# Kernel optimization log

Measured on AMD Instinct MI355X. Metric: run time of the kernel, lower is better.

The kernel has to match this reference:

```python
import jax, jax.numpy as jnp
import numpy as np

SAMPLING_RATE = 48000
HARMONIC_NUM = 8
DIM = HARMONIC_NUM + 1
SINE_AMP = 0.1
NOISE_STD = 0.003
VOICED_THRESHOLD = 0.0


def setup_inputs() -> dict:
    key = jax.random.key(0)
    B, T = 4, 480000
    # realistic voiced pitch contour in [80, 400) Hz
    f0 = jax.random.uniform(key, (B, T, 1), dtype=jnp.float32, minval=80.0, maxval=400.0)
    return {"f0": f0}


def reference(f0):
    B, T, _ = f0.shape
    # harmonic stack: f0_buf[:, :, k] = f0 * (k+1)   -> [B, T, DIM]
    harmonics = jnp.arange(1, DIM + 1, dtype=f0.dtype)
    f0_buf = f0 * harmonics  # broadcast [B,T,1] * [DIM]

    # normalized phase increment per sample
    rad_values = (f0_buf / SAMPLING_RATE) % 1.0

    # random initial phase per (batch, harmonic); fundamental gets phase 0
    k_ini, k_noise = jax.random.split(jax.random.key(42))
    rand_ini = jax.random.uniform(k_ini, (B, DIM), dtype=f0.dtype)
    rand_ini = rand_ini.at[:, 0].set(0.0)
    rad_values = rad_values.at[:, 0, :].add(rand_ini)

    # phase-unwrap correction: detect wrap points of cumsum % 1 and subtract 1
    tmp_over_one = jnp.cumsum(rad_values, axis=1) % 1.0
    wrap = (tmp_over_one[:, 1:, :] - tmp_over_one[:, :-1, :]) < 0  # [B,T-1,DIM]
    cumsum_shift = jnp.concatenate(
        [jnp.zeros((B, 1, DIM), dtype=f0.dtype), -wrap.astype(f0.dtype)], axis=1
    )

    phase = jnp.cumsum(rad_values + cumsum_shift, axis=1) * (2.0 * jnp.pi)
    sine_waves = jnp.sin(phase) * SINE_AMP  # [B,T,DIM]

    # voiced/unvoiced mask from fundamental f0
    uv = (f0 > VOICED_THRESHOLD).astype(f0.dtype)  # [B,T,1]

    noise_amp = uv * NOISE_STD + (1.0 - uv) * (SINE_AMP / 3.0)
    noise = jax.random.normal(k_noise, sine_waves.shape, dtype=f0.dtype)
    return sine_waves * uv + noise_amp * noise
```

## Files before the change

### kernel.cpp

```cpp
#include <hip/hip_runtime.h>
#include <math.h>
#include <stdint.h>

#pragma clang fp contract(off)

#define BB   4
#define TT   480000
#define DIM  9
#define TILE 256
#define NTT  1875

#define PARTITIONABLE 1

__host__ __device__ static inline void threefry2x32(uint32_t k0, uint32_t k1,
                                                    uint32_t x0, uint32_t x1,
                                                    uint32_t& o0, uint32_t& o1) {
  const uint32_t ks2 = k0 ^ k1 ^ 0x1BD11BDAu;
  x0 += k0; x1 += k1;
#define TF_R(r) { x0 += x1; x1 = (x1 << (r)) | (x1 >> (32 - (r))); x1 ^= x0; }
  TF_R(13) TF_R(15) TF_R(26) TF_R(6)
  x0 += k1;  x1 += ks2 + 1u;
  TF_R(17) TF_R(29) TF_R(16) TF_R(24)
  x0 += ks2; x1 += k0 + 2u;
  TF_R(13) TF_R(15) TF_R(26) TF_R(6)
  x0 += k0;  x1 += k1 + 3u;
  TF_R(17) TF_R(29) TF_R(16) TF_R(24)
  x0 += k1;  x1 += ks2 + 4u;
  TF_R(13) TF_R(15) TF_R(26) TF_R(6)
  x0 += ks2; x1 += k0 + 5u;
#undef TF_R
  o0 = x0; o1 = x1;
}

__device__ __forceinline__ float fracf_(float x) { return x - truncf(x); }

__device__ __forceinline__ float u01_(uint32_t bits) {
  return __uint_as_float((bits >> 9) | 0x3f800000u) - 1.0f;
}

__device__ static inline float erfinv_xla(float x) {
  float t = (1.0f - x) * (1.0f + x);
  float w = -0.6931471805599453f * __builtin_amdgcn_logf(t);
  float p;
  if (w < 5.0f) {
    w = w - 2.5f;
    p = 2.81022636e-08f;
    p = 3.43273939e-07f  + p * w;
    p = -3.5233877e-06f  + p * w;
    p = -4.39150654e-06f + p * w;
    p = 0.00021858087f   + p * w;
    p = -0.00125372503f  + p * w;
    p = -0.00417768164f  + p * w;
    p = 0.246640727f     + p * w;
    p = 1.50140941f      + p * w;
  } else {
    w = __builtin_amdgcn_sqrtf(w) - 3.0f;
    p = -0.000200214257f;
    p = 0.000100950558f  + p * w;
    p = 0.00134934322f   + p * w;
    p = -0.00367342844f  + p * w;
    p = 0.00573950773f   + p * w;
    p = -0.0076224613f   + p * w;
    p = 0.00943887047f   + p * w;
    p = 1.00167406f      + p * w;
    p = 2.83297682f      + p * w;
  }
  return p * x;
}

__device__ __forceinline__ float nrm_(uint32_t bits) {
  const float LO = -0.9999999403953552f;
  float u = u01_(bits) * 2.0f + LO;
  u = fmaxf(LO, u);
  return 1.4142135623730951f * erfinv_xla(u);
}

__device__ __forceinline__ uint32_t ri_bits(uint32_t kk0, uint32_t kk1, uint32_t j) {
  uint32_t o0, o1;
#if PARTITIONABLE
  threefry2x32(kk0, kk1, 0u, j, o0, o1);
  return o0 ^ o1;
#else
  if (j < 18u) { threefry2x32(kk0, kk1, j, j + 18u, o0, o1); return o0; }
  threefry2x32(kk0, kk1, j - 18u, j, o0, o1); return o1;
#endif
}

__device__ __forceinline__ uint32_t noise_bits(uint32_t kn0, uint32_t kn1, uint32_t i) {
  uint32_t o0, o1;
#if PARTITIONABLE
  threefry2x32(kn0, kn1, 0u, i, o0, o1);
  return o0 ^ o1;
#else
  const uint32_t half = 2u * TT * DIM;
  if (i < half) { threefry2x32(kn0, kn1, i, i + half, o0, o1); return o0; }
  threefry2x32(kn0, kn1, i - half, i, o0, o1); return o1;
#endif
}

__device__ __forceinline__ float rand_ini_val(uint32_t ki0, uint32_t ki1, int b, int k) {
  if (k == 0) return 0.0f;
  return u01_(ri_bits(ki0, ki1, (uint32_t)(b * DIM + k)));
}

struct Tree { float n1a, n1b, Mv[6]; };

__device__ __forceinline__ void build_tree4(float x0, float x1, float x2, float x3,
                                            Tree& T, int l) {
  T.n1a = x0 + x1;
  T.n1b = x2 + x3;
  T.Mv[0] = T.n1a + T.n1b;
#pragma unroll
  for (int s = 1; s < 6; ++s)
    T.Mv[s] = __shfl(T.Mv[s - 1], 2 * l) + __shfl(T.Mv[s - 1], 2 * l + 1);
}
__device__ __forceinline__ float tile_sum4(const Tree& T) {
  return __shfl(T.Mv[5], 0) + __shfl(T.Mv[5], 1);
}
__device__ __forceinline__ float fold4(const Tree& T, int n, float carry) {
  float acc = carry;
#pragma unroll
  for (int b = 7; b >= 2; --b) {
    float t = __shfl(T.Mv[b - 2], (n >> (b + 1)) << 1);
    acc = ((n >> b) & 1) ? acc + t : acc;
  }
  if (n & 2) acc = acc + T.n1a;
  return acc;
}

__global__ __launch_bounds__(256) void k_up1(const float* __restrict__ f0,
                                             float* __restrict__ gL,
                                             uint32_t ki0, uint32_t ki1) {
  int task = blockIdx.x * 4 + (threadIdx.x >> 6);
  int l = threadIdx.x & 63;
  int b = task / NTT, j = task - b * NTT;
  float4 f4 = *(const float4*)(f0 + (size_t)b * TT + j * TILE + 4 * l);
  const float RINV = 1.0f / 48000.0f;
  float rb0 = f4.x * RINV, rb1 = f4.y * RINV, rb2 = f4.z * RINV, rb3 = f4.w * RINV;
  bool ini = (j == 0) & (l == 0);
#pragma unroll
  for (int k = 0; k < DIM; ++k) {
    float h = (float)(k + 1);
    float r0 = fracf_(rb0 * h), r1 = fracf_(rb1 * h);
    float r2 = fracf_(rb2 * h), r3 = fracf_(rb3 * h);
    if (ini) r0 = r0 + rand_ini_val(ki0, ki1, b, k);
    Tree T; build_tree4(r0, r1, r2, r3, T, l);
    float ts = tile_sum4(T);
    if (l == 0) gL[(b * DIM + k) * NTT + j] = ts;
  }
}

__global__ __launch_bounds__(256) void k_midscan(float* __restrict__ gbuf) {
  const int NLEV = 11;
  const int SZ[11]  = {1875, 937, 468, 234, 117, 58, 29, 14, 7, 3, 1};
  const int OFF[11] = {0, 1875, 2812, 3280, 3514, 3631, 3689, 3718, 3732, 3739, 3742};
  __shared__ float buf[3743];
  float* g = gbuf + (size_t)blockIdx.x * NTT;
  int tid = threadIdx.x;
  float tmp[8];
#pragma unroll
  for (int u = 0; u < 8; ++u) { int i = tid + u * 256; tmp[u] = (i < NTT) ? g[i] : 0.0f; }
#pragma unroll
  for (int u = 0; u < 8; ++u) { int i = tid + u * 256; if (i < NTT) buf[i] = tmp[u]; }
  __syncthreads();
#pragma unroll
  for (int lv = 0; lv + 1 < NLEV; ++lv) {
    int m = SZ[lv + 1];
    const float* src = buf + OFF[lv];
    float* dst = buf + OFF[lv + 1];
    for (int i = tid; i < m; i += 256) dst[i] = src[2 * i] + src[2 * i + 1];
    __syncthreads();
  }
#pragma unroll
  for (int lv = NLEV - 2; lv >= 0; --lv) {
    int n = SZ[lv], m = SZ[lv + 1];
    float* cur = buf + OFF[lv];
    const float* up = buf + OFF[lv + 1];
    for (int i = tid; i < m; i += 256) {
      float s = up[i];
      cur[2 * i + 1] = s;
      if (2 * i + 2 < n) cur[2 * i + 2] = s + cur[2 * i + 2];
    }
    __syncthreads();
  }
#pragma unroll
  for (int u = 0; u < 8; ++u) { int i = tid + u * 256; if (i < NTT) g[i] = buf[i]; }
}

__global__ __launch_bounds__(256) void k_d1u2(const float* __restrict__ f0,
                                              const float* __restrict__ gS1,
                                              float* __restrict__ gL2,
                                              ulonglong2* __restrict__ wrapw,
                                              uint32_t ki0, uint32_t ki1) {
  int task = blockIdx.x * 4 + (threadIdx.x >> 6);
  int l = threadIdx.x & 63;
  int b = task / NTT, j = task - b * NTT;
  float4 f4 = *(const float4*)(f0 + (size_t)b * TT + j * TILE + 4 * l);
  const float RINV = 1.0f / 48000.0f;
  float rb0 = f4.x * RINV, rb1 = f4.y * RINV, rb2 = f4.z * RINV, rb3 = f4.w * RINV;
  bool ini = (j == 0) & (l == 0);
  bool notfirst = (j > 0) | (l > 0);
#pragma unroll
  for (int k = 0; k < DIM; ++k) {
    float h = (float)(k + 1);
    float r0 = fracf_(rb0 * h), r1 = fracf_(rb1 * h);
    float r2 = fracf_(rb2 * h), r3 = fracf_(rb3 * h);
    if (ini) r0 = r0 + rand_ini_val(ki0, ki1, b, k);
    Tree T; build_tree4(r0, r1, r2, r3, T, l);
    int base = (b * DIM + k) * NTT;
    float C = (j > 0) ? gS1[base + j - 1] : 0.0f;
    float S = gS1[base + j];
    float c3 = fold4(T, 4 * l + 4, C);
    c3 = (l == 63) ? S : c3;
    float c1 = fold4(T, 4 * l + 2, C);
    float cp = __shfl_up(c3, 1);
    if (l == 0) cp = C;
    float c0 = cp + r0;
    float c2 = c1 + r2;
    float fp = fracf_(cp), g0 = fracf_(c0), g1 = fracf_(c1);
    float g2 = fracf_(c2), g3 = fracf_(c3);
    bool w0 = notfirst & (g0 < fp);
    bool w1 = g1 < g0;
    bool w2 = g2 < g1;
    bool w3 = g3 < g2;
    float y0 = w0 ? r0 - 1.0f : r0, y1 = w1 ? r1 - 1.0f : r1;
    float y2 = w2 ? r2 - 1.0f : r2, y3 = w3 ? r3 - 1.0f : r3;
    unsigned long long m0 = __ballot(w0), m1 = __ballot(w1);
    unsigned long long m2 = __ballot(w2), m3 = __ballot(w3);
    Tree Ty; build_tree4(y0, y1, y2, y3, Ty, l);
    float ts = tile_sum4(Ty);
    if (l == 0) {
      gL2[base + j] = ts;
      wrapw[2 * (base + j)]     = make_ulonglong2(m0, m1);
      wrapw[2 * (base + j) + 1] = make_ulonglong2(m2, m3);
    }
  }
}

__global__ __launch_bounds__(256) void k_d2out(const float* __restrict__ f0,
                                               const float* __restrict__ gS2,
                                               const ulonglong2* __restrict__ wrapw,
                                               float* __restrict__ out,
                                               uint32_t ki0, uint32_t ki1,
                                               uint32_t kn0, uint32_t kn1) {
  int task = blockIdx.x * 4 + (threadIdx.x >> 6);
  int l = threadIdx.x & 63;
  int b = task / NTT, j = task - b * NTT;
  int t0 = j * TILE + 4 * l;
  float4 f4 = *(const float4*)(f0 + (size_t)b * TT + t0);
  const float RINV = 1.0f / 48000.0f;
  float rb0 = f4.x * RINV, rb1 = f4.y * RINV, rb2 = f4.z * RINV, rb3 = f4.w * RINV;
  bool ini = (j == 0) & (l == 0);
  float uv0 = (f4.x > 0.0f) ? 1.0f : 0.0f, uv1 = (f4.y > 0.0f) ? 1.0f : 0.0f;
  float uv2 = (f4.z > 0.0f) ? 1.0f : 0.0f, uv3 = (f4.w > 0.0f) ? 1.0f : 0.0f;
  const float AMP3 = 0.0333333333333333333f;
  float na0 = uv0 * 0.003f + (1.0f - uv0) * AMP3;
  float na1 = uv1 * 0.003f + (1.0f - uv1) * AMP3;
  float na2 = uv2 * 0.003f + (1.0f - uv2) * AMP3;
  float na3 = uv3 * 0.003f + (1.0f - uv3) * AMP3;
  float ob[36];
#pragma unroll
  for (int k = 0; k < DIM; ++k) {
    float h = (float)(k + 1);
    float r0 = fracf_(rb0 * h), r1 = fracf_(rb1 * h);
    float r2 = fracf_(rb2 * h), r3 = fracf_(rb3 * h);
    if (ini) r0 = r0 + rand_ini_val(ki0, ki1, b, k);
    int base = (b * DIM + k) * NTT;
    ulonglong2 wA = wrapw[2 * (base + j)];
    ulonglong2 wB = wrapw[2 * (base + j) + 1];
    float y0 = ((wA.x >> l) & 1ull) ? r0 - 1.0f : r0;
    float y1 = ((wA.y >> l) & 1ull) ? r1 - 1.0f : r1;
    float y2 = ((wB.x >> l) & 1ull) ? r2 - 1.0f : r2;
    float y3 = ((wB.y >> l) & 1ull) ? r3 - 1.0f : r3;
    Tree T; build_tree4(y0, y1, y2, y3, T, l);
    float C2 = (j > 0) ? gS2[base + j - 1] : 0.0f;
    float S2 = gS2[base + j];
    float d3 = fold4(T, 4 * l + 4, C2);
    d3 = (l == 63) ? S2 : d3;
    float d1 = fold4(T, 4 * l + 2, C2);
    float dp = __shfl_up(d3, 1);
    if (l == 0) dp = C2;
    float d0 = dp + y0;
    float d2 = d1 + y2;
    float s0 = __builtin_amdgcn_sinf(d0) * 0.1f;
    float s1 = __builtin_amdgcn_sinf(d1) * 0.1f;
    float s2 = __builtin_amdgcn_sinf(d2) * 0.1f;
    float s3 = __builtin_amdgcn_sinf(d3) * 0.1f;
    uint32_t fi = (uint32_t)(b * TT + t0) * (uint32_t)DIM + (uint32_t)k;
    float n0 = nrm_(noise_bits(kn0, kn1, fi));
    float n1 = nrm_(noise_bits(kn0, kn1, fi + 9u));
    float n2 = nrm_(noise_bits(kn0, kn1, fi + 18u));
    float n3 = nrm_(noise_bits(kn0, kn1, fi + 27u));
    ob[k]      = s0 * uv0 + na0 * n0;
    ob[9 + k]  = s1 * uv1 + na1 * n1;
    ob[18 + k] = s2 * uv2 + na2 * n2;
    ob[27 + k] = s3 * uv3 + na3 * n3;
  }
  float4* po = (float4*)(out + ((size_t)b * TT + t0) * DIM);
#pragma unroll
  for (int q = 0; q < 9; ++q)
    po[q] = make_float4(ob[4 * q], ob[4 * q + 1], ob[4 * q + 2], ob[4 * q + 3]);
}

extern "C" void kernel_launch(void* const* d_in, const int* in_sizes, int n_in,
                              void* d_out, int out_size, void* d_ws, size_t ws_size,
                              hipStream_t stream) {
  (void)in_sizes; (void)n_in; (void)out_size; (void)ws_size;
  const float* f0 = (const float*)d_in[0];
  float* out = (float*)d_out;
  float* gBuf1 = (float*)d_ws;
  float* gBuf2 = gBuf1 + 36 * NTT;
  ulonglong2* wrapw =
      (ulonglong2*)((char*)d_ws + (size_t)2 * 36 * NTT * sizeof(float));

  uint32_t ki0, ki1, kn0, kn1;
#if PARTITIONABLE
  threefry2x32(0u, 42u, 0u, 0u, ki0, ki1);
  threefry2x32(0u, 42u, 0u, 1u, kn0, kn1);
#else
  uint32_t a0, a1, b0, b1;
  threefry2x32(0u, 42u, 0u, 2u, a0, a1);
  threefry2x32(0u, 42u, 1u, 3u, b0, b1);
  ki0 = a0; ki1 = b0;
  kn0 = a1; kn1 = b1;
#endif

  k_up1    <<<(BB * NTT) / 4, 256, 0, stream>>>(f0, gBuf1, ki0, ki1);
  k_midscan<<<36, 256, 0, stream>>>(gBuf1);
  k_d1u2   <<<(BB * NTT) / 4, 256, 0, stream>>>(f0, gBuf1, gBuf2, wrapw, ki0, ki1);
  k_midscan<<<36, 256, 0, stream>>>(gBuf2);
  k_d2out  <<<(BB * NTT) / 4, 256, 0, stream>>>(f0, gBuf2, wrapw, out,
                                                ki0, ki1, kn0, kn1);
}
```

Measured before the change: 197.4 us.

## Stage output through LDS for coalesced stores and use wave-per-row midscan

The output kernel now writes each wave's 256×9 results into padded shared memory and then stores them as contiguous float4 runs across lanes. Before, each lane wrote 36 consecutive floats, which gave strided per-lane stores. The mid-level scan now gives one wave per row (9 blocks of 4 waves instead of 36 blocks), which removes block-wide barriers. Scalar readfirstlane indexing and an inline v_cndmask that consumes the wrap bitmask directly as an SGPR lane mask shorten the wrap-bit select. The trade-offs are more LDS use per block in the output kernel and fewer workgroups in the scan, and the wave-synchronous scan leans on lockstep wave execution without any barrier.

```diff
diff --git a/kernel.cpp b/kernel.cpp
--- a/kernel.cpp
+++ b/kernel.cpp
@@ -103,6 +103,12 @@
   return u01_(ri_bits(ki0, ki1, (uint32_t)(b * DIM + k)));
 }
 
+__device__ __forceinline__ float selbit(unsigned long long m, float aFalse, float bTrue) {
+  float r;
+  asm("v_cndmask_b32 %0, %1, %2, %3" : "=v"(r) : "v"(aFalse), "v"(bTrue), "s"(m));
+  return r;
+}
+
 struct Tree { float n1a, n1b, Mv[6]; };
 
 __device__ __forceinline__ void build_tree4(float x0, float x1, float x2, float x3,
@@ -154,37 +160,31 @@
   const int NLEV = 11;
   const int SZ[11]  = {1875, 937, 468, 234, 117, 58, 29, 14, 7, 3, 1};
   const int OFF[11] = {0, 1875, 2812, 3280, 3514, 3631, 3689, 3718, 3732, 3739, 3742};
-  __shared__ float buf[3743];
-  float* g = gbuf + (size_t)blockIdx.x * NTT;
-  int tid = threadIdx.x;
-  float tmp[8];
-#pragma unroll
-  for (int u = 0; u < 8; ++u) { int i = tid + u * 256; tmp[u] = (i < NTT) ? g[i] : 0.0f; }
-#pragma unroll
-  for (int u = 0; u < 8; ++u) { int i = tid + u * 256; if (i < NTT) buf[i] = tmp[u]; }
-  __syncthreads();
+  __shared__ float buf[4][3743];
+  int w = threadIdx.x >> 6, l = threadIdx.x & 63;
+  int row = blockIdx.x * 4 + w;
+  float* g = gbuf + (size_t)row * NTT;
+  float* s = buf[w];
+  for (int i = l; i < NTT; i += 64) s[i] = g[i];
 #pragma unroll
   for (int lv = 0; lv + 1 < NLEV; ++lv) {
     int m = SZ[lv + 1];
-    const float* src = buf + OFF[lv];
-    float* dst = buf + OFF[lv + 1];
-    for (int i = tid; i < m; i += 256) dst[i] = src[2 * i] + src[2 * i + 1];
-    __syncthreads();
+    const float* src = s + OFF[lv];
+    float* dst = s + OFF[lv + 1];
+    for (int i = l; i < m; i += 64) dst[i] = src[2 * i] + src[2 * i + 1];
   }
 #pragma unroll
   for (int lv = NLEV - 2; lv >= 0; --lv) {
     int n = SZ[lv], m = SZ[lv + 1];
-    float* cur = buf + OFF[lv];
-    const float* up = buf + OFF[lv + 1];
-    for (int i = tid; i < m; i += 256) {
-      float s = up[i];
-      cur[2 * i + 1] = s;
-      if (2 * i + 2 < n) cur[2 * i + 2] = s + cur[2 * i + 2];
+    float* cur = s + OFF[lv];
+    const float* up = s + OFF[lv + 1];
+    for (int i = l; i < m; i += 64) {
+      float ss = up[i];
+      cur[2 * i + 1] = ss;
+      if (2 * i + 2 < n) cur[2 * i + 2] = ss + cur[2 * i + 2];
     }
-    __syncthreads();
-  }
-#pragma unroll
-  for (int u = 0; u < 8; ++u) { int i = tid + u * 256; if (i < NTT) g[i] = buf[i]; }
+  }
+  for (int i = l; i < NTT; i += 64) g[i] = s[i];
 }
 
 __global__ __launch_bounds__(256) void k_d1u2(const float* __restrict__ f0,
@@ -207,9 +207,9 @@
     float r2 = fracf_(rb2 * h), r3 = fracf_(rb3 * h);
     if (ini) r0 = r0 + rand_ini_val(ki0, ki1, b, k);
     Tree T; build_tree4(r0, r1, r2, r3, T, l);
-    int base = (b * DIM + k) * NTT;
-    float C = (j > 0) ? gS1[base + j - 1] : 0.0f;
-    float S = gS1[base + j];
+    int bju = __builtin_amdgcn_readfirstlane((b * DIM + k) * NTT + j);
+    float S = gS1[bju];
+    float C = (j > 0) ? gS1[bju - 1] : 0.0f;
     float c3 = fold4(T, 4 * l + 4, C);
     c3 = (l == 63) ? S : c3;
     float c1 = fold4(T, 4 * l + 2, C);
@@ -230,9 +230,9 @@
     Tree Ty; build_tree4(y0, y1, y2, y3, Ty, l);
     float ts = tile_sum4(Ty);
     if (l == 0) {
-      gL2[base + j] = ts;
-      wrapw[2 * (base + j)]     = make_ulonglong2(m0, m1);
-      wrapw[2 * (base + j) + 1] = make_ulonglong2(m2, m3);
+      gL2[bju] = ts;
+      wrapw[2 * (size_t)bju]     = make_ulonglong2(m0, m1);
+      wrapw[2 * (size_t)bju + 1] = make_ulonglong2(m2, m3);
     }
   }
 }
@@ -243,8 +243,9 @@
                                                float* __restrict__ out,
                                                uint32_t ki0, uint32_t ki1,
                                                uint32_t kn0, uint32_t kn1) {
-  int task = blockIdx.x * 4 + (threadIdx.x >> 6);
-  int l = threadIdx.x & 63;
+  __shared__ float sb[4][64 * 37];
+  int w = threadIdx.x >> 6, l = threadIdx.x & 63;
+  int task = blockIdx.x * 4 + w;
   int b = task / NTT, j = task - b * NTT;
   int t0 = j * TILE + 4 * l;
   float4 f4 = *(const float4*)(f0 + (size_t)b * TT + t0);
@@ -258,23 +259,24 @@
   float na1 = uv1 * 0.003f + (1.0f - uv1) * AMP3;
   float na2 = uv2 * 0.003f + (1.0f - uv2) * AMP3;
   float na3 = uv3 * 0.003f + (1.0f - uv3) * AMP3;
-  float ob[36];
+  float* sl = sb[w];
+  int sbase = l * 37;
 #pragma unroll
   for (int k = 0; k < DIM; ++k) {
     float h = (float)(k + 1);
     float r0 = fracf_(rb0 * h), r1 = fracf_(rb1 * h);
     float r2 = fracf_(rb2 * h), r3 = fracf_(rb3 * h);
     if (ini) r0 = r0 + rand_ini_val(ki0, ki1, b, k);
-    int base = (b * DIM + k) * NTT;
-    ulonglong2 wA = wrapw[2 * (base + j)];
-    ulonglong2 wB = wrapw[2 * (base + j) + 1];
-    float y0 = ((wA.x >> l) & 1ull) ? r0 - 1.0f : r0;
-    float y1 = ((wA.y >> l) & 1ull) ? r1 - 1.0f : r1;
-    float y2 = ((wB.x >> l) & 1ull) ? r2 - 1.0f : r2;
-    float y3 = ((wB.y >> l) & 1ull) ? r3 - 1.0f : r3;
+    int bju = __builtin_amdgcn_readfirstlane((b * DIM + k) * NTT + j);
+    ulonglong2 wA = wrapw[2 * (size_t)bju];
+    ulonglong2 wB = wrapw[2 * (size_t)bju + 1];
+    float S2 = gS2[bju];
+    float C2 = (j > 0) ? gS2[bju - 1] : 0.0f;
+    float y0 = selbit(wA.x, r0, r0 - 1.0f);
+    float y1 = selbit(wA.y, r1, r1 - 1.0f);
+    float y2 = selbit(wB.x, r2, r2 - 1.0f);
+    float y3 = selbit(wB.y, r3, r3 - 1.0f);
     Tree T; build_tree4(y0, y1, y2, y3, T, l);
-    float C2 = (j > 0) ? gS2[base + j - 1] : 0.0f;
-    float S2 = gS2[base + j];
     float d3 = fold4(T, 4 * l + 4, C2);
     d3 = (l == 63) ? S2 : d3;
     float d1 = fold4(T, 4 * l + 2, C2);
@@ -291,15 +293,19 @@
     float n1 = nrm_(noise_bits(kn0, kn1, fi + 9u));
     float n2 = nrm_(noise_bits(kn0, kn1, fi + 18u));
     float n3 = nrm_(noise_bits(kn0, kn1, fi + 27u));
-    ob[k]      = s0 * uv0 + na0 * n0;
-    ob[9 + k]  = s1 * uv1 + na1 * n1;
-    ob[18 + k] = s2 * uv2 + na2 * n2;
-    ob[27 + k] = s3 * uv3 + na3 * n3;
-  }
-  float4* po = (float4*)(out + ((size_t)b * TT + t0) * DIM);
-#pragma unroll
-  for (int q = 0; q < 9; ++q)
-    po[q] = make_float4(ob[4 * q], ob[4 * q + 1], ob[4 * q + 2], ob[4 * q + 3]);
+    sl[sbase + k]      = s0 * uv0 + na0 * n0;
+    sl[sbase + 9 + k]  = s1 * uv1 + na1 * n1;
+    sl[sbase + 18 + k] = s2 * uv2 + na2 * n2;
+    sl[sbase + 27 + k] = s3 * uv3 + na3 * n3;
+  }
+  float4* po = (float4*)(out + ((size_t)b * TT + (size_t)j * TILE) * DIM);
+#pragma unroll
+  for (int q = 0; q < 9; ++q) {
+    int gg = (q * 64 + l) * 4;
+    int a = gg + gg / 36;
+    float4 v = make_float4(sl[a], sl[a + 1], sl[a + 2], sl[a + 3]);
+    po[q * 64 + l] = v;
+  }
 }
 
 extern "C" void kernel_launch(void* const* d_in, const int* in_sizes, int n_in,
@@ -326,9 +332,9 @@
 #endif
 
   k_up1    <<<(BB * NTT) / 4, 256, 0, stream>>>(f0, gBuf1, ki0, ki1);
-  k_midscan<<<36, 256, 0, stream>>>(gBuf1);
+  k_midscan<<<9, 256, 0, stream>>>(gBuf1);
   k_d1u2   <<<(BB * NTT) / 4, 256, 0, stream>>>(f0, gBuf1, gBuf2, wrapw, ki0, ki1);
-  k_midscan<<<36, 256, 0, stream>>>(gBuf2);
+  k_midscan<<<9, 256, 0, stream>>>(gBuf2);
   k_d2out  <<<(BB * NTT) / 4, 256, 0, stream>>>(f0, gBuf2, wrapw, out,
                                                 ki0, ki1, kn0, kn1);
 }
```

After: 179.3 us. 1.1x faster.
